# Kernel tuning notes

Measured on AMD Instinct MI355X. Metric: run time of the kernel, lower is better.

Reference implementation:

```python
import jax, jax.numpy as jnp
import numpy as np

N_NODES = 100000
N_EDGES = 800000
D_IN = 128
D_HID = 128
N_CLASSES = 64


def _glorot(key, shape):
    fan_in, fan_out = shape[0], shape[1]
    lim = jnp.sqrt(6.0 / (fan_in + fan_out)).astype(jnp.float32)
    return jax.random.uniform(key, shape, jnp.float32, -lim, lim)


def setup_inputs() -> dict:
    key = jax.random.key(0)
    ks = jax.random.split(key, 20)
    inp = {
        "x": jax.random.normal(ks[0], (N_NODES, D_IN), jnp.float32),
        "edge_src": jax.random.randint(ks[1], (N_EDGES,), 0, N_NODES, jnp.int32),
        "edge_dst": jax.random.randint(ks[2], (N_EDGES,), 0, N_NODES, jnp.int32),
    }
    dims = [(D_IN, D_HID), (D_HID, D_HID), (D_HID, N_CLASSES)]
    k = 3
    for i, (di, do) in enumerate(dims):
        inp[f"Wp{i}"] = _glorot(ks[k], (di, di)); k += 1   # fc_pool: d_in -> d_in
        inp[f"bp{i}"] = jnp.zeros((di,), jnp.float32)
        inp[f"Ws{i}"] = _glorot(ks[k], (di, do)); k += 1   # fc_self (no bias)
        inp[f"Wn{i}"] = _glorot(ks[k], (di, do)); k += 1   # fc_neigh
        inp[f"bn{i}"] = jnp.zeros((do,), jnp.float32)
    return inp


def _sage_pool_layer(x, src, dst, Wp, bp, Ws, Wn, bn):
    # pool aggregator: max over in-edges of relu(fc_pool(h_src))
    m = jax.nn.relu(x @ Wp + bp)                 # [N, d_in]
    msg = m[src]                                 # [E, d_in] gather
    agg = jax.ops.segment_max(msg, dst, num_segments=N_NODES)  # scatter-max
    agg = jnp.where(jnp.isfinite(agg), agg, 0.0)  # zero-in-degree nodes -> 0
    return x @ Ws + agg @ Wn + bn


def reference(x, edge_src, edge_dst,
              Wp0, bp0, Ws0, Wn0, bn0,
              Wp1, bp1, Ws1, Wn1, bn1,
              Wp2, bp2, Ws2, Wn2, bn2):
    layers = [
        (Wp0, bp0, Ws0, Wn0, bn0),
        (Wp1, bp1, Ws1, Wn1, bn1),
        (Wp2, bp2, Ws2, Wn2, bn2),
    ]
    h = x
    for (Wp, bp, Ws, Wn, bn) in layers:
        # SAGEConv internal activation=relu followed by wrapper F.relu (idempotent)
        h = jax.nn.relu(_sage_pool_layer(h, edge_src, edge_dst, Wp, bp, Ws, Wn, bn))
    return jax.nn.log_softmax(h, axis=-1)
```

## Files before the change

### kernel.cpp

```cpp
#include <hip/hip_runtime.h>
#include <cstddef>
#include <cstdint>

#define NNODES 100000
#define NEDGES 800000
#define CAP 32
#define NXCD 8
#define NPB (NNODES / NXCD)
#define BINCAP 110592

typedef unsigned short u16;
typedef __attribute__((ext_vector_type(8))) short short8;
typedef __attribute__((ext_vector_type(8))) _Float16 half8;
typedef __attribute__((ext_vector_type(4))) float f32x4;
typedef __attribute__((ext_vector_type(4))) int int4v;

__device__ __forceinline__ u16 f32_to_bf16(float f) {
    union { float f; uint32_t u; } v; v.f = f;
    uint32_t r = v.u + 0x7FFF + ((v.u >> 16) & 1);
    return (u16)(r >> 16);
}
__device__ __forceinline__ u16 f32_to_f16(float f) {
    union { _Float16 h; u16 u; } v; v.h = (_Float16)f;
    return v.u;
}
__device__ __forceinline__ uint32_t pkmax(uint32_t a, uint32_t b) {
    uint32_t lo = max(a & 0xFFFFu, b & 0xFFFFu);
    uint32_t hi = max(a >> 16, b >> 16);
    return lo | (hi << 16);
}

__global__ __launch_bounds__(256) void zero_kernel(float4* __restrict__ p, int n4) {
    int i = blockIdx.x * blockDim.x + threadIdx.x;
    const int stride = gridDim.x * blockDim.x;
    for (; i < n4; i += stride) p[i] = make_float4(0.f, 0.f, 0.f, 0.f);
}

__global__ __launch_bounds__(256) void bin_kernel(
    const int* __restrict__ src, const int* __restrict__ dst,
    int* __restrict__ gcnt, int* __restrict__ bind, int* __restrict__ bins, int E)
{
    __shared__ int ld[1024], ls[1024];
    __shared__ int lcnt[8], lpre[8], lgb[8];
    const int tid = threadIdx.x;
    const int base = blockIdx.x * 1024;

    if (tid < 8) lcnt[tid] = 0;
    __syncthreads();

    int d[4], s[4], slot[4], b[4];
    int nv = 0;
    if (base + tid * 4 + 3 < E) {
        const int4v dd = *(const int4v*)&dst[base + tid * 4];
        const int4v ss = *(const int4v*)&src[base + tid * 4];
#pragma unroll
        for (int j = 0; j < 4; ++j) { d[j] = dd[j]; s[j] = ss[j]; }
        nv = 4;
    } else {
        for (int j = 0; j < 4; ++j) {
            const int idx = base + tid * 4 + j;
            if (idx < E) { d[nv] = dst[idx]; s[nv] = src[idx]; ++nv; }
        }
    }
#pragma unroll 4
    for (int j = 0; j < nv; ++j) {
        b[j] = d[j] / NPB;
        slot[j] = atomicAdd(&lcnt[b[j]], 1);
    }
    __syncthreads();
    if (tid == 0) {
        int run = 0;
#pragma unroll
        for (int k = 0; k < 8; ++k) { lpre[k] = run; run += lcnt[k]; }
    }
    __syncthreads();
#pragma unroll 4
    for (int j = 0; j < nv; ++j) {
        const int p = lpre[b[j]] + slot[j];
        ld[p] = d[j]; ls[p] = s[j];
    }
    if (tid < 8 && lcnt[tid] > 0) lgb[tid] = atomicAdd(&gcnt[tid], lcnt[tid]);
    __syncthreads();
    const int total = lpre[7] + lcnt[7];
    for (int i = tid; i < total; i += 256) {
        const int d_ = ld[i];
        const int b_ = d_ / NPB;
        const int g = lgb[b_] + (i - lpre[b_]);
        if (g < BINCAP) {
            bind[b_ * BINCAP + g] = d_;
            bins[b_ * BINCAP + g] = ls[i];
        }
    }
}

__global__ __launch_bounds__(256) void scatter_fill_kernel(
    const int* __restrict__ gcnt,
    const int* __restrict__ bind, const int* __restrict__ bins,
    int* __restrict__ deg, int* __restrict__ col2)
{
    const int xcd  = blockIdx.x & (NXCD - 1);
    const int grp  = blockIdx.x >> 3;
    const int ngrp = gridDim.x >> 3;
    int cnt = gcnt[xcd]; if (cnt > BINCAP) cnt = BINCAP;
    const int* bd = bind + xcd * BINCAP;
    const int* bs = bins + xcd * BINCAP;
    for (int i = grp * 256 + threadIdx.x; i < cnt; i += ngrp * 256) {
        const int d = bd[i];
        const int r = atomicAdd(&deg[d], 1);
        if (r < CAP) col2[d * CAP + r] = bs[i];
    }
}

__global__ __launch_bounds__(256) void bf16_cast_kernel(
    const float4* __restrict__ in, uint2* __restrict__ out, int n4)
{
    int i = blockIdx.x * 256 + threadIdx.x;
    const int stride = gridDim.x * 256;
    for (; i < n4; i += stride) {
        float4 v = in[i];
        out[i] = make_uint2(
            (uint32_t)f32_to_bf16(v.x) | ((uint32_t)f32_to_bf16(v.y) << 16),
            (uint32_t)f32_to_bf16(v.z) | ((uint32_t)f32_to_bf16(v.w) << 16));
    }
}

struct WPtrs { const float* w[9]; };

__global__ __launch_bounds__(256) void split_weights_kernel(WPtrs p, u16* __restrict__ wbase)
{
    const int idx = blockIdx.x * 256 + threadIdx.x;
    const int w = blockIdx.y;
    const int DO_ = (w >= 7) ? 64 : 128;
    if (idx >= 128 * DO_) return;
    const float v = p.w[w][idx];
    const int k = idx / DO_;
    const int c = idx - k * DO_;
    const bool use_f16 = (w == 2 || w == 5 || w == 8);
    wbase[w * 32768 + c * 128 + k] = use_f16 ? f32_to_f16(v) : f32_to_bf16(v);
}

__global__ __launch_bounds__(256) void copy_w_kernel(
    const uint32_t* __restrict__ w7, const uint32_t* __restrict__ w8,
    uint32_t* __restrict__ dstw)
{
    int i = blockIdx.x * 256 + threadIdx.x;
    if (i < 4096) dstw[i] = w7[i];
    else if (i < 8192) dstw[i] = w8[i - 4096];
}

template<int DO, bool DUAL, int OUT_MODE>
__global__ __launch_bounds__(512, 4) void mfma_gemm_kernel(
    const u16* __restrict__ A,
    const u16* __restrict__ Cq,
    const u16* __restrict__ WaT, const u16* __restrict__ WbT,
    const float* __restrict__ bias,
    float* __restrict__ outF, u16* __restrict__ outU,
    int N)
{
    constexpr int CT = DO / 16;
    constexpr int WS = 136;
    __shared__ u16 sW[(DUAL ? 2 : 1) * DO * WS];

    const int tid = threadIdx.x;

    for (int i = tid; i < DO * 16; i += 512) {
        const int r = i >> 4;
        const int c = (i & 15) << 3;
        *(short8*)&sW[r * WS + c] = *(const short8*)&WaT[r * 128 + c];
        if constexpr (DUAL)
            *(short8*)&sW[DO * WS + r * WS + c] = *(const short8*)&WbT[r * 128 + c];
    }

    const int lane = tid & 63;
    const int wid  = tid >> 6;
    const int l15  = lane & 15;
    const int lk   = (lane >> 4) << 3;
    const int row0 = blockIdx.x * 256 + wid * 32;

    int aoff0, aoff1;
    {
        int r0 = row0 + l15;      if (r0 > N - 1) r0 = N - 1;
        int r1 = row0 + 16 + l15; if (r1 > N - 1) r1 = N - 1;
        aoff0 = r0 * 128 + lk;
        aoff1 = r1 * 128 + lk;
    }

    f32x4 acc[2][CT];
#pragma unroll
    for (int m = 0; m < 2; ++m)
#pragma unroll
        for (int c = 0; c < CT; ++c) acc[m][c] = (f32x4){0.f, 0.f, 0.f, 0.f};

    __syncthreads();

#pragma unroll
    for (int k = 0; k < 4; ++k) {
        const int ko = 32 * k;
        short8 ah0 = *(const short8*)(A + aoff0 + ko);
        short8 ah1 = *(const short8*)(A + aoff1 + ko);
        half8 ch0, ch1;
        if constexpr (DUAL) {
            ch0 = *(const half8*)(Cq + aoff0 + ko);
            ch1 = *(const half8*)(Cq + aoff1 + ko);
        }
#pragma unroll
        for (int ct = 0; ct < CT; ++ct) {
            const int wb = (ct * 16 + l15) * WS + lk + ko;
            short8 wh = *(const short8*)&sW[wb];
            acc[0][ct] = __builtin_amdgcn_mfma_f32_16x16x32_bf16(ah0, wh, acc[0][ct], 0, 0, 0);
            acc[1][ct] = __builtin_amdgcn_mfma_f32_16x16x32_bf16(ah1, wh, acc[1][ct], 0, 0, 0);
            if constexpr (DUAL) {
                half8 vh = *(const half8*)&sW[DO * WS + wb];
                acc[0][ct] = __builtin_amdgcn_mfma_f32_16x16x32_f16(ch0, vh, acc[0][ct], 0, 0, 0);
                acc[1][ct] = __builtin_amdgcn_mfma_f32_16x16x32_f16(ch1, vh, acc[1][ct], 0, 0, 0);
            }
        }
    }

    float bv[CT];
#pragma unroll
    for (int ct = 0; ct < CT; ++ct) bv[ct] = bias[ct * 16 + l15];

    const int jrow = (lane >> 4) << 2;
#pragma unroll
    for (int m = 0; m < 2; ++m) {
#pragma unroll
        for (int j = 0; j < 4; ++j) {
            const int r = row0 + m * 16 + jrow + j;
            if constexpr (OUT_MODE == 3) {
                float v[CT];
                float mx = 0.f;
#pragma unroll
                for (int ct = 0; ct < CT; ++ct) {
                    v[ct] = fmaxf(acc[m][ct][j] + bv[ct], 0.f);
                    mx = fmaxf(mx, v[ct]);
                }
#pragma unroll
                for (int off = 1; off < 16; off <<= 1) mx = fmaxf(mx, __shfl_xor(mx, off));
                float s = 0.f;
#pragma unroll
                for (int ct = 0; ct < CT; ++ct) s += __expf(v[ct] - mx);
#pragma unroll
                for (int off = 1; off < 16; off <<= 1) s += __shfl_xor(s, off);
                const float lse = mx + __logf(s);
                if (r < N) {
#pragma unroll
                    for (int ct = 0; ct < CT; ++ct)
                        outF[(size_t)r * DO + ct * 16 + l15] = v[ct] - lse;
                }
            } else if (r < N) {
#pragma unroll
                for (int ct = 0; ct < CT; ++ct) {
                    float v = fmaxf(acc[m][ct][j] + bv[ct], 0.f);
                    const size_t o = (size_t)r * DO + ct * 16 + l15;
                    if constexpr (OUT_MODE == 0) {
                        outF[o] = v;
                    } else if constexpr (OUT_MODE == 1) {
                        outU[o] = f32_to_bf16(v);
                    } else if constexpr (OUT_MODE == 2) {
                        outU[o] = f32_to_f16(v);
                    }
                }
            }
        }
    }
}

__global__ __launch_bounds__(256) void aggregate_kernel(
    const uint4* __restrict__ m4,
    const int* __restrict__ deg,
    const int* __restrict__ col2,
    uint4* __restrict__ agg4, int N)
{
    const int tid  = threadIdx.x;
    const int l16  = tid & 15;
    const int node = (blockIdx.x * 256 + tid) >> 4;
    if (node >= N) return;
    int cnt = deg[node];
    if (cnt > CAP) cnt = CAP;
    const int base = node * CAP;

    uint32_t a0 = 0, a1 = 0, a2 = 0, a3 = 0;
    int e = 0;
    for (; e + 4 <= cnt; e += 4) {
        const int s0 = col2[base + e],     s1 = col2[base + e + 1];
        const int s2 = col2[base + e + 2], s3 = col2[base + e + 3];
        const uint4 v0 = m4[(size_t)s0 * 16 + l16];
        const uint4 v1 = m4[(size_t)s1 * 16 + l16];
        const uint4 v2 = m4[(size_t)s2 * 16 + l16];
        const uint4 v3 = m4[(size_t)s3 * 16 + l16];
        a0 = pkmax(a0, v0.x); a1 = pkmax(a1, v0.y); a2 = pkmax(a2, v0.z); a3 = pkmax(a3, v0.w);
        a0 = pkmax(a0, v1.x); a1 = pkmax(a1, v1.y); a2 = pkmax(a2, v1.z); a3 = pkmax(a3, v1.w);
        a0 = pkmax(a0, v2.x); a1 = pkmax(a1, v2.y); a2 = pkmax(a2, v2.z); a3 = pkmax(a3, v2.w);
        a0 = pkmax(a0, v3.x); a1 = pkmax(a1, v3.y); a2 = pkmax(a2, v3.z); a3 = pkmax(a3, v3.w);
    }
    for (; e < cnt; ++e) {
        const uint4 v0 = m4[(size_t)col2[base + e] * 16 + l16];
        a0 = pkmax(a0, v0.x); a1 = pkmax(a1, v0.y); a2 = pkmax(a2, v0.z); a3 = pkmax(a3, v0.w);
    }
    agg4[(size_t)node * 16 + l16] = make_uint4(a0, a1, a2, a3);
}

extern "C" void kernel_launch(void* const* d_in, const int* in_sizes, int n_in,
                              void* d_out, int out_size, void* d_ws, size_t ws_size,
                              hipStream_t stream)
{
    const int N = NNODES, E = NEDGES;
    const float* x  = (const float*)d_in[0];
    const int* esrc = (const int*)d_in[1];
    const int* edst = (const int*)d_in[2];
    const float* bp[3] = {(const float*)d_in[4], (const float*)d_in[9],  (const float*)d_in[14]};
    const float* bn[3] = {(const float*)d_in[7], (const float*)d_in[12], (const float*)d_in[17]};

    char* ws = (char*)d_ws;
    const size_t P = (size_t)N * 128 * 2;
    u16* p0 = (u16*)(ws);
    u16* p2 = (u16*)(ws + 2 * P);
    u16* p4 = (u16*)(ws + 4 * P);
    u16* p5 = (u16*)(ws + 5 * P);

    char* ob = (char*)d_out;
    int* deg    = (int*)ob;
    int* gcnt   = (int*)(ob + 400000);
    int* col2   = (int*)(ob + 409600);
    u16* wbase  = (u16*)(ob + 409600 + (size_t)N * CAP * 4);
    int* bind   = (int*)(ob + 13800448);
    int* bins   = (int*)(ob + 13800448 + 8 * BINCAP * 4);
    auto WT = [&](int i) { return wbase + i * 32768; };

    const int gblocks = (N + 255) / 256;
    const int ablocks = (N * 16 + 255) / 256;
    const int bblocks = (E + 1023) / 1024;
    dim3 blk(256), gblk(512);

    zero_kernel<<<128, blk, 0, stream>>>((float4*)ob, 409600 / 16);
    bin_kernel<<<bblocks, blk, 0, stream>>>(esrc, edst, gcnt, bind, bins, E);
    scatter_fill_kernel<<<2048, blk, 0, stream>>>(gcnt, bind, bins, deg, col2);

    WPtrs wp;
    wp.w[0] = (const float*)d_in[3];  wp.w[1] = (const float*)d_in[5];  wp.w[2] = (const float*)d_in[6];
    wp.w[3] = (const float*)d_in[8];  wp.w[4] = (const float*)d_in[10]; wp.w[5] = (const float*)d_in[11];
    wp.w[6] = (const float*)d_in[13]; wp.w[7] = (const float*)d_in[15]; wp.w[8] = (const float*)d_in[16];
    split_weights_kernel<<<dim3(64, 9), blk, 0, stream>>>(wp, wbase);
    bf16_cast_kernel<<<2048, blk, 0, stream>>>((const float4*)x, (uint2*)p0, N * 128 / 4);

    mfma_gemm_kernel<128, false, 2><<<gblocks, gblk, 0, stream>>>(
        p0, nullptr, WT(0), nullptr, bp[0], nullptr, p4, N);
    aggregate_kernel<<<ablocks, blk, 0, stream>>>((const uint4*)p4, deg, col2, (uint4*)p5, N);
    mfma_gemm_kernel<128, true, 1><<<gblocks, gblk, 0, stream>>>(
        p0, p5, WT(1), WT(2), bn[0], nullptr, p2, N);

    mfma_gemm_kernel<128, false, 2><<<gblocks, gblk, 0, stream>>>(
        p2, nullptr, WT(3), nullptr, bp[1], nullptr, p4, N);
    aggregate_kernel<<<ablocks, blk, 0, stream>>>((const uint4*)p4, deg, col2, (uint4*)p5, N);
    mfma_gemm_kernel<128, true, 1><<<gblocks, gblk, 0, stream>>>(
        p2, p5, WT(4), WT(5), bn[1], nullptr, p0, N);

    mfma_gemm_kernel<128, false, 2><<<gblocks, gblk, 0, stream>>>(
        p0, nullptr, WT(6), nullptr, bp[2], nullptr, p4, N);
    aggregate_kernel<<<ablocks, blk, 0, stream>>>((const uint4*)p4, deg, col2, (uint4*)p5, N);
    copy_w_kernel<<<32, blk, 0, stream>>>((const uint32_t*)WT(7), (const uint32_t*)WT(8), (uint32_t*)p4);
    mfma_gemm_kernel<64, true, 3><<<gblocks, gblk, 0, stream>>>(
        p0, p5, p4, p4 + 8192, bn[2], (float*)d_out, nullptr, N);
}
```

Before: 271.5 us.

## Fuse neighbor max-aggregation into dual GEMM and cast x in-kernel

The separate aggregate kernel is removed. Each dual GEMM now gathers the neighbor fp16 messages and applies packed max directly in registers, then uses the result as the second MFMA operand, so the aggregated buffer no longer makes a round trip through global memory. The first layer's GEMMs read fp32 x and convert to bf16 in registers, which drops the cast kernel, and the weight copy kernel is dropped by moving the scratch buffers into the workspace. Dual GEMM blocks now cover 128 rows each, doubling their grid, and the irregular gather latency now sits inside the MFMA kernel, which may hurt overlap.

```diff
diff --git a/kernel.cpp b/kernel.cpp
--- a/kernel.cpp
+++ b/kernel.cpp
@@ -28,6 +28,31 @@
     uint32_t lo = max(a & 0xFFFFu, b & 0xFFFFu);
     uint32_t hi = max(a >> 16, b >> 16);
     return lo | (hi << 16);
+}
+__device__ __forceinline__ void agmax(uint4& a, uint4 v) {
+    a.x = pkmax(a.x, v.x); a.y = pkmax(a.y, v.y);
+    a.z = pkmax(a.z, v.z); a.w = pkmax(a.w, v.w);
+}
+
+__device__ __forceinline__ void gather_row(
+    uint4 (&ag)[4], const uint4* __restrict__ m4,
+    const int* __restrict__ deg, const int* __restrict__ col2, int row, int sec)
+{
+    int cnt = deg[row]; if (cnt > CAP) cnt = CAP;
+    const int base = row * CAP;
+    int e = 0;
+    for (; e + 2 <= cnt; e += 2) {
+        const uint4* q0 = m4 + (size_t)col2[base + e] * 16 + sec;
+        const uint4* q1 = m4 + (size_t)col2[base + e + 1] * 16 + sec;
+        uint4 v00 = q0[0], v01 = q0[4], v02 = q0[8], v03 = q0[12];
+        uint4 v10 = q1[0], v11 = q1[4], v12 = q1[8], v13 = q1[12];
+        agmax(ag[0], v00); agmax(ag[1], v01); agmax(ag[2], v02); agmax(ag[3], v03);
+        agmax(ag[0], v10); agmax(ag[1], v11); agmax(ag[2], v12); agmax(ag[3], v13);
+    }
+    if (e < cnt) {
+        const uint4* q0 = m4 + (size_t)col2[base + e] * 16 + sec;
+        agmax(ag[0], q0[0]); agmax(ag[1], q0[4]); agmax(ag[2], q0[8]); agmax(ag[3], q0[12]);
+    }
 }
 
 __global__ __launch_bounds__(256) void zero_kernel(float4* __restrict__ p, int n4) {
@@ -111,19 +136,6 @@
     }
 }
 
-__global__ __launch_bounds__(256) void bf16_cast_kernel(
-    const float4* __restrict__ in, uint2* __restrict__ out, int n4)
-{
-    int i = blockIdx.x * 256 + threadIdx.x;
-    const int stride = gridDim.x * 256;
-    for (; i < n4; i += stride) {
-        float4 v = in[i];
-        out[i] = make_uint2(
-            (uint32_t)f32_to_bf16(v.x) | ((uint32_t)f32_to_bf16(v.y) << 16),
-            (uint32_t)f32_to_bf16(v.z) | ((uint32_t)f32_to_bf16(v.w) << 16));
-    }
-}
-
 struct WPtrs { const float* w[9]; };
 
 __global__ __launch_bounds__(256) void split_weights_kernel(WPtrs p, u16* __restrict__ wbase)
@@ -139,25 +151,17 @@
     wbase[w * 32768 + c * 128 + k] = use_f16 ? f32_to_f16(v) : f32_to_bf16(v);
 }
 
-__global__ __launch_bounds__(256) void copy_w_kernel(
-    const uint32_t* __restrict__ w7, const uint32_t* __restrict__ w8,
-    uint32_t* __restrict__ dstw)
-{
-    int i = blockIdx.x * 256 + threadIdx.x;
-    if (i < 4096) dstw[i] = w7[i];
-    else if (i < 8192) dstw[i] = w8[i - 4096];
-}
-
-template<int DO, bool DUAL, int OUT_MODE>
+template<int DO, bool DUAL, int OUT_MODE, bool AF32>
 __global__ __launch_bounds__(512, 4) void mfma_gemm_kernel(
-    const u16* __restrict__ A,
-    const u16* __restrict__ Cq,
+    const void* __restrict__ Av,
+    const int* __restrict__ deg, const int* __restrict__ col2,
+    const uint4* __restrict__ m4,
     const u16* __restrict__ WaT, const u16* __restrict__ WbT,
     const float* __restrict__ bias,
-    float* __restrict__ outF, u16* __restrict__ outU,
-    int N)
+    float* __restrict__ outF, u16* __restrict__ outU, int N)
 {
     constexpr int CT = DO / 16;
+    constexpr int MT = DUAL ? 1 : 2;
     constexpr int WS = 136;
     __shared__ u16 sW[(DUAL ? 2 : 1) * DO * WS];
 
@@ -174,20 +178,32 @@
     const int lane = tid & 63;
     const int wid  = tid >> 6;
     const int l15  = lane & 15;
-    const int lk   = (lane >> 4) << 3;
-    const int row0 = blockIdx.x * 256 + wid * 32;
-
-    int aoff0, aoff1;
-    {
-        int r0 = row0 + l15;      if (r0 > N - 1) r0 = N - 1;
-        int r1 = row0 + 16 + l15; if (r1 > N - 1) r1 = N - 1;
-        aoff0 = r0 * 128 + lk;
-        aoff1 = r1 * 128 + lk;
-    }
-
-    f32x4 acc[2][CT];
-#pragma unroll
-    for (int m = 0; m < 2; ++m)
+    const int sec  = lane >> 4;
+    const int lk   = sec << 3;
+    const int row0 = blockIdx.x * (128 * MT) + wid * (16 * MT);
+
+    int rc[MT], aoff[MT];
+#pragma unroll
+    for (int m = 0; m < MT; ++m) {
+        int r = row0 + m * 16 + l15; if (r > N - 1) r = N - 1;
+        rc[m] = r;
+        aoff[m] = r * 128 + lk;
+    }
+
+    uint4 ag[MT][4];
+    if constexpr (DUAL) {
+#pragma unroll
+        for (int m = 0; m < MT; ++m)
+#pragma unroll
+            for (int k = 0; k < 4; ++k) ag[m][k] = make_uint4(0, 0, 0, 0);
+#pragma unroll
+        for (int m = 0; m < MT; ++m)
+            gather_row(ag[m], m4, deg, col2, rc[m], sec);
+    }
+
+    f32x4 acc[MT][CT];
+#pragma unroll
+    for (int m = 0; m < MT; ++m)
 #pragma unroll
         for (int c = 0; c < CT; ++c) acc[m][c] = (f32x4){0.f, 0.f, 0.f, 0.f};
 
@@ -196,23 +212,42 @@
 #pragma unroll
     for (int k = 0; k < 4; ++k) {
         const int ko = 32 * k;
-        short8 ah0 = *(const short8*)(A + aoff0 + ko);
-        short8 ah1 = *(const short8*)(A + aoff1 + ko);
-        half8 ch0, ch1;
+        short8 ah[MT];
+#pragma unroll
+        for (int m = 0; m < MT; ++m) {
+            if constexpr (AF32) {
+                const float* pa = (const float*)Av + aoff[m] + ko;
+                f32x4 a = *(const f32x4*)pa;
+                f32x4 b = *(const f32x4*)(pa + 4);
+#pragma unroll
+                for (int j = 0; j < 4; ++j) {
+                    ah[m][j]     = (short)f32_to_bf16(a[j]);
+                    ah[m][j + 4] = (short)f32_to_bf16(b[j]);
+                }
+            } else {
+                ah[m] = *(const short8*)((const u16*)Av + aoff[m] + ko);
+            }
+        }
+        half8 ch[MT];
         if constexpr (DUAL) {
-            ch0 = *(const half8*)(Cq + aoff0 + ko);
-            ch1 = *(const half8*)(Cq + aoff1 + ko);
+#pragma unroll
+            for (int m = 0; m < MT; ++m) {
+                union { uint4 u; half8 h; } t; t.u = ag[m][k];
+                ch[m] = t.h;
+            }
         }
 #pragma unroll
         for (int ct = 0; ct < CT; ++ct) {
             const int wb = (ct * 16 + l15) * WS + lk + ko;
             short8 wh = *(const short8*)&sW[wb];
-            acc[0][ct] = __builtin_amdgcn_mfma_f32_16x16x32_bf16(ah0, wh, acc[0][ct], 0, 0, 0);
-            acc[1][ct] = __builtin_amdgcn_mfma_f32_16x16x32_bf16(ah1, wh, acc[1][ct], 0, 0, 0);
+#pragma unroll
+            for (int m = 0; m < MT; ++m)
+                acc[m][ct] = __builtin_amdgcn_mfma_f32_16x16x32_bf16(ah[m], wh, acc[m][ct], 0, 0, 0);
             if constexpr (DUAL) {
                 half8 vh = *(const half8*)&sW[DO * WS + wb];
-                acc[0][ct] = __builtin_amdgcn_mfma_f32_16x16x32_f16(ch0, vh, acc[0][ct], 0, 0, 0);
-                acc[1][ct] = __builtin_amdgcn_mfma_f32_16x16x32_f16(ch1, vh, acc[1][ct], 0, 0, 0);
+#pragma unroll
+                for (int m = 0; m < MT; ++m)
+                    acc[m][ct] = __builtin_amdgcn_mfma_f32_16x16x32_f16(ch[m], vh, acc[m][ct], 0, 0, 0);
             }
         }
     }
@@ -221,9 +256,9 @@
 #pragma unroll
     for (int ct = 0; ct < CT; ++ct) bv[ct] = bias[ct * 16 + l15];
 
-    const int jrow = (lane >> 4) << 2;
-#pragma unroll
-    for (int m = 0; m < 2; ++m) {
+    const int jrow = sec << 2;
+#pragma unroll
+    for (int m = 0; m < MT; ++m) {
 #pragma unroll
         for (int j = 0; j < 4; ++j) {
             const int r = row0 + m * 16 + jrow + j;
@@ -253,52 +288,15 @@
                 for (int ct = 0; ct < CT; ++ct) {
                     float v = fmaxf(acc[m][ct][j] + bv[ct], 0.f);
                     const size_t o = (size_t)r * DO + ct * 16 + l15;
-                    if constexpr (OUT_MODE == 0) {
-                        outF[o] = v;
-                    } else if constexpr (OUT_MODE == 1) {
+                    if constexpr (OUT_MODE == 1) {
                         outU[o] = f32_to_bf16(v);
-                    } else if constexpr (OUT_MODE == 2) {
+                    } else {
                         outU[o] = f32_to_f16(v);
                     }
                 }
             }
         }
     }
-}
-
-__global__ __launch_bounds__(256) void aggregate_kernel(
-    const uint4* __restrict__ m4,
-    const int* __restrict__ deg,
-    const int* __restrict__ col2,
-    uint4* __restrict__ agg4, int N)
-{
-    const int tid  = threadIdx.x;
-    const int l16  = tid & 15;
-    const int node = (blockIdx.x * 256 + tid) >> 4;
-    if (node >= N) return;
-    int cnt = deg[node];
-    if (cnt > CAP) cnt = CAP;
-    const int base = node * CAP;
-
-    uint32_t a0 = 0, a1 = 0, a2 = 0, a3 = 0;
-    int e = 0;
-    for (; e + 4 <= cnt; e += 4) {
-        const int s0 = col2[base + e],     s1 = col2[base + e + 1];
-        const int s2 = col2[base + e + 2], s3 = col2[base + e + 3];
-        const uint4 v0 = m4[(size_t)s0 * 16 + l16];
-        const uint4 v1 = m4[(size_t)s1 * 16 + l16];
-        const uint4 v2 = m4[(size_t)s2 * 16 + l16];
-        const uint4 v3 = m4[(size_t)s3 * 16 + l16];
-        a0 = pkmax(a0, v0.x); a1 = pkmax(a1, v0.y); a2 = pkmax(a2, v0.z); a3 = pkmax(a3, v0.w);
-        a0 = pkmax(a0, v1.x); a1 = pkmax(a1, v1.y); a2 = pkmax(a2, v1.z); a3 = pkmax(a3, v1.w);
-        a0 = pkmax(a0, v2.x); a1 = pkmax(a1, v2.y); a2 = pkmax(a2, v2.z); a3 = pkmax(a3, v2.w);
-        a0 = pkmax(a0, v3.x); a1 = pkmax(a1, v3.y); a2 = pkmax(a2, v3.z); a3 = pkmax(a3, v3.w);
-    }
-    for (; e < cnt; ++e) {
-        const uint4 v0 = m4[(size_t)col2[base + e] * 16 + l16];
-        a0 = pkmax(a0, v0.x); a1 = pkmax(a1, v0.y); a2 = pkmax(a2, v0.z); a3 = pkmax(a3, v0.w);
-    }
-    agg4[(size_t)node * 16 + l16] = make_uint4(a0, a1, a2, a3);
 }
 
 extern "C" void kernel_launch(void* const* d_in, const int* in_sizes, int n_in,
@@ -315,25 +313,26 @@
     char* ws = (char*)d_ws;
     const size_t P = (size_t)N * 128 * 2;
     u16* p0 = (u16*)(ws);
+    char* p1 = ws + P;
     u16* p2 = (u16*)(ws + 2 * P);
+    char* p3 = ws + 3 * P;
     u16* p4 = (u16*)(ws + 4 * P);
     u16* p5 = (u16*)(ws + 5 * P);
 
-    char* ob = (char*)d_out;
-    int* deg    = (int*)ob;
-    int* gcnt   = (int*)(ob + 400000);
-    int* col2   = (int*)(ob + 409600);
-    u16* wbase  = (u16*)(ob + 409600 + (size_t)N * CAP * 4);
-    int* bind   = (int*)(ob + 13800448);
-    int* bins   = (int*)(ob + 13800448 + 8 * BINCAP * 4);
+    int* deg  = (int*)p1;
+    int* gcnt = (int*)(p1 + 400000);
+    int* col2 = (int*)(p1 + 409600);
+    int* bind = (int*)p3;
+    int* bins = bind + 8 * BINCAP;
+    u16* wbase = p5;
     auto WT = [&](int i) { return wbase + i * 32768; };
 
-    const int gblocks = (N + 255) / 256;
-    const int ablocks = (N * 16 + 255) / 256;
+    const int gs = (N + 255) / 256;
+    const int gd = (N + 127) / 128;
     const int bblocks = (E + 1023) / 1024;
     dim3 blk(256), gblk(512);
 
-    zero_kernel<<<128, blk, 0, stream>>>((float4*)ob, 409600 / 16);
+    zero_kernel<<<128, blk, 0, stream>>>((float4*)p1, 409600 / 16);
     bin_kernel<<<bblocks, blk, 0, stream>>>(esrc, edst, gcnt, bind, bins, E);
     scatter_fill_kernel<<<2048, blk, 0, stream>>>(gcnt, bind, bins, deg, col2);
 
@@ -342,24 +341,19 @@
     wp.w[3] = (const float*)d_in[8];  wp.w[4] = (const float*)d_in[10]; wp.w[5] = (const float*)d_in[11];
     wp.w[6] = (const float*)d_in[13]; wp.w[7] = (const float*)d_in[15]; wp.w[8] = (const float*)d_in[16];
     split_weights_kernel<<<dim3(64, 9), blk, 0, stream>>>(wp, wbase);
-    bf16_cast_kernel<<<2048, blk, 0, stream>>>((const float4*)x, (uint2*)p0, N * 128 / 4);
-
-    mfma_gemm_kernel<128, false, 2><<<gblocks, gblk, 0, stream>>>(
-        p0, nullptr, WT(0), nullptr, bp[0], nullptr, p4, N);
-    aggregate_kernel<<<ablocks, blk, 0, stream>>>((const uint4*)p4, deg, col2, (uint4*)p5, N);
-    mfma_gemm_kernel<128, true, 1><<<gblocks, gblk, 0, stream>>>(
-        p0, p5, WT(1), WT(2), bn[0], nullptr, p2, N);
-
-    mfma_gemm_kernel<128, false, 2><<<gblocks, gblk, 0, stream>>>(
-        p2, nullptr, WT(3), nullptr, bp[1], nullptr, p4, N);
-    aggregate_kernel<<<ablocks, blk, 0, stream>>>((const uint4*)p4, deg, col2, (uint4*)p5, N);
-    mfma_gemm_kernel<128, true, 1><<<gblocks, gblk, 0, stream>>>(
-        p2, p5, WT(4), WT(5), bn[1], nullptr, p0, N);
-
-    mfma_gemm_kernel<128, false, 2><<<gblocks, gblk, 0, stream>>>(
-        p0, nullptr, WT(6), nullptr, bp[2], nullptr, p4, N);
-    aggregate_kernel<<<ablocks, blk, 0, stream>>>((const uint4*)p4, deg, col2, (uint4*)p5, N);
-    copy_w_kernel<<<32, blk, 0, stream>>>((const uint32_t*)WT(7), (const uint32_t*)WT(8), (uint32_t*)p4);
-    mfma_gemm_kernel<64, true, 3><<<gblocks, gblk, 0, stream>>>(
-        p0, p5, p4, p4 + 8192, bn[2], (float*)d_out, nullptr, N);
-}
+
+    mfma_gemm_kernel<128, false, 2, true><<<gs, gblk, 0, stream>>>(
+        x, nullptr, nullptr, nullptr, WT(0), nullptr, bp[0], nullptr, p4, N);
+    mfma_gemm_kernel<128, true, 1, true><<<gd, gblk, 0, stream>>>(
+        x, deg, col2, (const uint4*)p4, WT(1), WT(2), bn[0], nullptr, p2, N);
+
+    mfma_gemm_kernel<128, false, 2, false><<<gs, gblk, 0, stream>>>(
+        p2, nullptr, nullptr, nullptr, WT(3), nullptr, bp[1], nullptr, p4, N);
+    mfma_gemm_kernel<128, true, 1, false><<<gd, gblk, 0, stream>>>(
+        p2, deg, col2, (const uint4*)p4, WT(4), WT(5), bn[1], nullptr, p0, N);
+
+    mfma_gemm_kernel<128, false, 2, false><<<gs, gblk, 0, stream>>>(
+        p0, nullptr, nullptr, nullptr, WT(6), nullptr, bp[2], nullptr, p4, N);
+    mfma_gemm_kernel<64, true, 3, false><<<gd, gblk, 0, stream>>>(
+        p0, deg, col2, (const uint4*)p4, WT(7), WT(8), bn[2], (float*)d_out, nullptr, N);
+}
```

Result: no change. 269.7 us, median of 3 (-0.7%).

## Fuse fp32-to-bf16 input cast into GEMM, halve GEMM row tile, move scratch to workspace

Applied to the files above, without the earlier changes.

Removes the standalone bf16 cast pass over x by having the first-layer GEMMs load fp32 rows and convert them to bf16 in registers. It also removes the weight copy kernel by moving the graph scratch buffers and weights out of the output buffer into the workspace. Each wave now computes 16 rows instead of 32, doubling the grid size and lowering register use. The tradeoff is that x is read twice in fp32 (more bytes), and weights are reloaded into shared memory by twice as many blocks.

```diff
diff --git a/kernel.cpp b/kernel.cpp
--- a/kernel.cpp
+++ b/kernel.cpp
@@ -111,19 +111,6 @@
     }
 }
 
-__global__ __launch_bounds__(256) void bf16_cast_kernel(
-    const float4* __restrict__ in, uint2* __restrict__ out, int n4)
-{
-    int i = blockIdx.x * 256 + threadIdx.x;
-    const int stride = gridDim.x * 256;
-    for (; i < n4; i += stride) {
-        float4 v = in[i];
-        out[i] = make_uint2(
-            (uint32_t)f32_to_bf16(v.x) | ((uint32_t)f32_to_bf16(v.y) << 16),
-            (uint32_t)f32_to_bf16(v.z) | ((uint32_t)f32_to_bf16(v.w) << 16));
-    }
-}
-
 struct WPtrs { const float* w[9]; };
 
 __global__ __launch_bounds__(256) void split_weights_kernel(WPtrs p, u16* __restrict__ wbase)
@@ -137,133 +124,6 @@
     const int c = idx - k * DO_;
     const bool use_f16 = (w == 2 || w == 5 || w == 8);
     wbase[w * 32768 + c * 128 + k] = use_f16 ? f32_to_f16(v) : f32_to_bf16(v);
-}
-
-__global__ __launch_bounds__(256) void copy_w_kernel(
-    const uint32_t* __restrict__ w7, const uint32_t* __restrict__ w8,
-    uint32_t* __restrict__ dstw)
-{
-    int i = blockIdx.x * 256 + threadIdx.x;
-    if (i < 4096) dstw[i] = w7[i];
-    else if (i < 8192) dstw[i] = w8[i - 4096];
-}
-
-template<int DO, bool DUAL, int OUT_MODE>
-__global__ __launch_bounds__(512, 4) void mfma_gemm_kernel(
-    const u16* __restrict__ A,
-    const u16* __restrict__ Cq,
-    const u16* __restrict__ WaT, const u16* __restrict__ WbT,
-    const float* __restrict__ bias,
-    float* __restrict__ outF, u16* __restrict__ outU,
-    int N)
-{
-    constexpr int CT = DO / 16;
-    constexpr int WS = 136;
-    __shared__ u16 sW[(DUAL ? 2 : 1) * DO * WS];
-
-    const int tid = threadIdx.x;
-
-    for (int i = tid; i < DO * 16; i += 512) {
-        const int r = i >> 4;
-        const int c = (i & 15) << 3;
-        *(short8*)&sW[r * WS + c] = *(const short8*)&WaT[r * 128 + c];
-        if constexpr (DUAL)
-            *(short8*)&sW[DO * WS + r * WS + c] = *(const short8*)&WbT[r * 128 + c];
-    }
-
-    const int lane = tid & 63;
-    const int wid  = tid >> 6;
-    const int l15  = lane & 15;
-    const int lk   = (lane >> 4) << 3;
-    const int row0 = blockIdx.x * 256 + wid * 32;
-
-    int aoff0, aoff1;
-    {
-        int r0 = row0 + l15;      if (r0 > N - 1) r0 = N - 1;
-        int r1 = row0 + 16 + l15; if (r1 > N - 1) r1 = N - 1;
-        aoff0 = r0 * 128 + lk;
-        aoff1 = r1 * 128 + lk;
-    }
-
-    f32x4 acc[2][CT];
-#pragma unroll
-    for (int m = 0; m < 2; ++m)
-#pragma unroll
-        for (int c = 0; c < CT; ++c) acc[m][c] = (f32x4){0.f, 0.f, 0.f, 0.f};
-
-    __syncthreads();
-
-#pragma unroll
-    for (int k = 0; k < 4; ++k) {
-        const int ko = 32 * k;
-        short8 ah0 = *(const short8*)(A + aoff0 + ko);
-        short8 ah1 = *(const short8*)(A + aoff1 + ko);
-        half8 ch0, ch1;
-        if constexpr (DUAL) {
-            ch0 = *(const half8*)(Cq + aoff0 + ko);
-            ch1 = *(const half8*)(Cq + aoff1 + ko);
-        }
-#pragma unroll
-        for (int ct = 0; ct < CT; ++ct) {
-            const int wb = (ct * 16 + l15) * WS + lk + ko;
-            short8 wh = *(const short8*)&sW[wb];
-            acc[0][ct] = __builtin_amdgcn_mfma_f32_16x16x32_bf16(ah0, wh, acc[0][ct], 0, 0, 0);
-            acc[1][ct] = __builtin_amdgcn_mfma_f32_16x16x32_bf16(ah1, wh, acc[1][ct], 0, 0, 0);
-            if constexpr (DUAL) {
-                half8 vh = *(const half8*)&sW[DO * WS + wb];
-                acc[0][ct] = __builtin_amdgcn_mfma_f32_16x16x32_f16(ch0, vh, acc[0][ct], 0, 0, 0);
-                acc[1][ct] = __builtin_amdgcn_mfma_f32_16x16x32_f16(ch1, vh, acc[1][ct], 0, 0, 0);
-            }
-        }
-    }
-
-    float bv[CT];
-#pragma unroll
-    for (int ct = 0; ct < CT; ++ct) bv[ct] = bias[ct * 16 + l15];
-
-    const int jrow = (lane >> 4) << 2;
-#pragma unroll
-    for (int m = 0; m < 2; ++m) {
-#pragma unroll
-        for (int j = 0; j < 4; ++j) {
-            const int r = row0 + m * 16 + jrow + j;
-            if constexpr (OUT_MODE == 3) {
-                float v[CT];
-                float mx = 0.f;
-#pragma unroll
-                for (int ct = 0; ct < CT; ++ct) {
-                    v[ct] = fmaxf(acc[m][ct][j] + bv[ct], 0.f);
-                    mx = fmaxf(mx, v[ct]);
-                }
-#pragma unroll
-                for (int off = 1; off < 16; off <<= 1) mx = fmaxf(mx, __shfl_xor(mx, off));
-                float s = 0.f;
-#pragma unroll
-                for (int ct = 0; ct < CT; ++ct) s += __expf(v[ct] - mx);
-#pragma unroll
-                for (int off = 1; off < 16; off <<= 1) s += __shfl_xor(s, off);
-                const float lse = mx + __logf(s);
-                if (r < N) {
-#pragma unroll
-                    for (int ct = 0; ct < CT; ++ct)
-                        outF[(size_t)r * DO + ct * 16 + l15] = v[ct] - lse;
-                }
-            } else if (r < N) {
-#pragma unroll
-                for (int ct = 0; ct < CT; ++ct) {
-                    float v = fmaxf(acc[m][ct][j] + bv[ct], 0.f);
-                    const size_t o = (size_t)r * DO + ct * 16 + l15;
-                    if constexpr (OUT_MODE == 0) {
-                        outF[o] = v;
-                    } else if constexpr (OUT_MODE == 1) {
-                        outU[o] = f32_to_bf16(v);
-                    } else if constexpr (OUT_MODE == 2) {
-                        outU[o] = f32_to_f16(v);
-                    }
-                }
-            }
-        }
-    }
 }
 
 __global__ __launch_bounds__(256) void aggregate_kernel(
@@ -301,6 +161,121 @@
     agg4[(size_t)node * 16 + l16] = make_uint4(a0, a1, a2, a3);
 }
 
+template<int DO, bool DUAL, int OUT_MODE, bool AF32>
+__global__ __launch_bounds__(512, 4) void mfma_gemm_kernel(
+    const void* __restrict__ Av,
+    const u16* __restrict__ Cq,
+    const u16* __restrict__ WaT, const u16* __restrict__ WbT,
+    const float* __restrict__ bias,
+    float* __restrict__ outF, u16* __restrict__ outU, int N)
+{
+    constexpr int CT = DO / 16;
+    constexpr int WS = 136;
+    __shared__ u16 sW[(DUAL ? 2 : 1) * DO * WS];
+
+    const int tid = threadIdx.x;
+
+    for (int i = tid; i < DO * 16; i += 512) {
+        const int r = i >> 4;
+        const int c = (i & 15) << 3;
+        *(short8*)&sW[r * WS + c] = *(const short8*)&WaT[r * 128 + c];
+        if constexpr (DUAL)
+            *(short8*)&sW[DO * WS + r * WS + c] = *(const short8*)&WbT[r * 128 + c];
+    }
+
+    const int lane = tid & 63;
+    const int wid  = tid >> 6;
+    const int l15  = lane & 15;
+    const int sec  = lane >> 4;
+    const int lk   = sec << 3;
+    const int row0 = blockIdx.x * 128 + wid * 16;
+
+    int aoff;
+    {
+        int r = row0 + l15; if (r > N - 1) r = N - 1;
+        aoff = r * 128 + lk;
+    }
+
+    f32x4 acc[CT];
+#pragma unroll
+    for (int c = 0; c < CT; ++c) acc[c] = (f32x4){0.f, 0.f, 0.f, 0.f};
+
+    __syncthreads();
+
+#pragma unroll
+    for (int k = 0; k < 4; ++k) {
+        const int ko = 32 * k;
+        short8 ah;
+        if constexpr (AF32) {
+            const float* pa = (const float*)Av + aoff + ko;
+            f32x4 a = *(const f32x4*)pa;
+            f32x4 b = *(const f32x4*)(pa + 4);
+#pragma unroll
+            for (int j = 0; j < 4; ++j) {
+                ah[j]     = (short)f32_to_bf16(a[j]);
+                ah[j + 4] = (short)f32_to_bf16(b[j]);
+            }
+        } else {
+            ah = *(const short8*)((const u16*)Av + aoff + ko);
+        }
+        half8 ch;
+        if constexpr (DUAL) ch = *(const half8*)(Cq + aoff + ko);
+#pragma unroll
+        for (int ct = 0; ct < CT; ++ct) {
+            const int wb = (ct * 16 + l15) * WS + lk + ko;
+            short8 wh = *(const short8*)&sW[wb];
+            acc[ct] = __builtin_amdgcn_mfma_f32_16x16x32_bf16(ah, wh, acc[ct], 0, 0, 0);
+            if constexpr (DUAL) {
+                half8 vh = *(const half8*)&sW[DO * WS + wb];
+                acc[ct] = __builtin_amdgcn_mfma_f32_16x16x32_f16(ch, vh, acc[ct], 0, 0, 0);
+            }
+        }
+    }
+
+    float bv[CT];
+#pragma unroll
+    for (int ct = 0; ct < CT; ++ct) bv[ct] = bias[ct * 16 + l15];
+
+    const int jrow = sec << 2;
+#pragma unroll
+    for (int j = 0; j < 4; ++j) {
+        const int r = row0 + jrow + j;
+        if constexpr (OUT_MODE == 3) {
+            float v[CT];
+            float mx = 0.f;
+#pragma unroll
+            for (int ct = 0; ct < CT; ++ct) {
+                v[ct] = fmaxf(acc[ct][j] + bv[ct], 0.f);
+                mx = fmaxf(mx, v[ct]);
+            }
+#pragma unroll
+            for (int off = 1; off < 16; off <<= 1) mx = fmaxf(mx, __shfl_xor(mx, off));
+            float s = 0.f;
+#pragma unroll
+            for (int ct = 0; ct < CT; ++ct) s += __expf(v[ct] - mx);
+#pragma unroll
+            for (int off = 1; off < 16; off <<= 1) s += __shfl_xor(s, off);
+            const float lse = mx + __logf(s);
+            if (r < N) {
+#pragma unroll
+                for (int ct = 0; ct < CT; ++ct)
+                    outF[(size_t)r * DO + ct * 16 + l15] = v[ct] - lse;
+            }
+        } else if (r < N) {
+#pragma unroll
+            for (int ct = 0; ct < CT; ++ct) {
+                float v = fmaxf(acc[ct][j] + bv[ct], 0.f);
+                const size_t o = (size_t)r * DO + ct * 16 + l15;
+                if constexpr (OUT_MODE == 1) {
+                    outU[o] = f32_to_bf16(v);
+                } else {
+                    outU[o] = f32_to_f16(v);
+                }
+            }
+        }
+    }
+}
+
 extern "C" void kernel_launch(void* const* d_in, const int* in_sizes, int n_in,
                               void* d_out, int out_size, void* d_ws, size_t ws_size,
                               hipStream_t stream)
@@ -315,25 +290,26 @@
     char* ws = (char*)d_ws;
     const size_t P = (size_t)N * 128 * 2;
     u16* p0 = (u16*)(ws);
+    char* p1 = ws + P;
     u16* p2 = (u16*)(ws + 2 * P);
+    char* p3 = ws + 3 * P;
     u16* p4 = (u16*)(ws + 4 * P);
     u16* p5 = (u16*)(ws + 5 * P);
-
-    char* ob = (char*)d_out;
-    int* deg    = (int*)ob;
-    int* gcnt   = (int*)(ob + 400000);
-    int* col2   = (int*)(ob + 409600);
-    u16* wbase  = (u16*)(ob + 409600 + (size_t)N * CAP * 4);
-    int* bind   = (int*)(ob + 13800448);
-    int* bins   = (int*)(ob + 13800448 + 8 * BINCAP * 4);
+    u16* wbase = (u16*)(p3 + 2 * 8 * BINCAP * 4 + 4096);
+
+    int* deg  = (int*)p1;
+    int* gcnt = (int*)(p1 + 400000);
+    int* col2 = (int*)(p1 + 409600);
+    int* bind = (int*)p3;
+    int* bins = bind + 8 * BINCAP;
     auto WT = [&](int i) { return wbase + i * 32768; };
 
-    const int gblocks = (N + 255) / 256;
+    const int gg = (N + 127) / 128;
     const int ablocks = (N * 16 + 255) / 256;
     const int bblocks = (E + 1023) / 1024;
     dim3 blk(256), gblk(512);
 
-    zero_kernel<<<128, blk, 0, stream>>>((float4*)ob, 409600 / 16);
+    zero_kernel<<<128, blk, 0, stream>>>((float4*)p1, 409600 / 16);
     bin_kernel<<<bblocks, blk, 0, stream>>>(esrc, edst, gcnt, bind, bins, E);
     scatter_fill_kernel<<<2048, blk, 0, stream>>>(gcnt, bind, bins, deg, col2);
 
@@ -342,24 +318,22 @@
     wp.w[3] = (const float*)d_in[8];  wp.w[4] = (const float*)d_in[10]; wp.w[5] = (const float*)d_in[11];
     wp.w[6] = (const float*)d_in[13]; wp.w[7] = (const float*)d_in[15]; wp.w[8] = (const float*)d_in[16];
     split_weights_kernel<<<dim3(64, 9), blk, 0, stream>>>(wp, wbase);
-    bf16_cast_kernel<<<2048, blk, 0, stream>>>((const float4*)x, (uint2*)p0, N * 128 / 4);
-
-    mfma_gemm_kernel<128, false, 2><<<gblocks, gblk, 0, stream>>>(
-        p0, nullptr, WT(0), nullptr, bp[0], nullptr, p4, N);
+
+    mfma_gemm_kernel<128, false, 2, true><<<gg, gblk, 0, stream>>>(
+        x, nullptr, WT(0), nullptr, bp[0], nullptr, p4, N);
     aggregate_kernel<<<ablocks, blk, 0, stream>>>((const uint4*)p4, deg, col2, (uint4*)p5, N);
-    mfma_gemm_kernel<128, true, 1><<<gblocks, gblk, 0, stream>>>(
-        p0, p5, WT(1), WT(2), bn[0], nullptr, p2, N);
-
-    mfma_gemm_kernel<128, false, 2><<<gblocks, gblk, 0, stream>>>(
+    mfma_gemm_kernel<128, true, 1, true><<<gg, gblk, 0, stream>>>(
+        x, p5, WT(1), WT(2), bn[0], nullptr, p2, N);
+
+    mfma_gemm_kernel<128, false, 2, false><<<gg, gblk, 0, stream>>>(
         p2, nullptr, WT(3), nullptr, bp[1], nullptr, p4, N);
     aggregate_kernel<<<ablocks, blk, 0, stream>>>((const uint4*)p4, deg, col2, (uint4*)p5, N);
-    mfma_gemm_kernel<128, true, 1><<<gblocks, gblk, 0, stream>>>(
+    mfma_gemm_kernel<128, true, 1, false><<<gg, gblk, 0, stream>>>(
         p2, p5, WT(4), WT(5), bn[1], nullptr, p0, N);
 
-    mfma_gemm_kernel<128, false, 2><<<gblocks, gblk, 0, stream>>>(
+    mfma_gemm_kernel<128, false, 2, false><<<gg, gblk, 0, stream>>>(
         p0, nullptr, WT(6), nullptr, bp[2], nullptr, p4, N);
     aggregate_kernel<<<ablocks, blk, 0, stream>>>((const uint4*)p4, deg, col2, (uint4*)p5, N);
-    copy_w_kernel<<<32, blk, 0, stream>>>((const uint32_t*)WT(7), (const uint32_t*)WT(8), (uint32_t*)p4);
-    mfma_gemm_kernel<64, true, 3><<<gblocks, gblk, 0, stream>>>(
-        p0, p5, p4, p4 + 8192, bn[2], (float*)d_out, nullptr, N);
-}
+    mfma_gemm_kernel<64, true, 3, false><<<gg, gblk, 0, stream>>>(
+        p0, p5, WT(7), WT(8), bn[2], (float*)d_out, nullptr, N);
+}
```

New measurement: 272.1 us. No clear change (+0.2%).
